# Optimization experiments

Hardware: AMD Instinct MI355X
Metric: run time of the kernel (lower is better)

## Reference

```python
import jax, jax.numpy as jnp
import numpy as np
from jax import lax

B, S, HID, H, HKV, D, M = 2, 4096, 2048, 16, 8, 128, 256
CHUNK = 128
EPS = 1e-6


def setup_inputs() -> dict:
    key = jax.random.key(0)
    ks = jax.random.split(key, 6)
    hidden_states = jax.random.normal(ks[0], (B, S, HID), jnp.float32)
    wq = jax.random.normal(ks[1], (H * D, HID), jnp.float32) / np.sqrt(HID)
    wk = jax.random.normal(ks[2], (HKV * D, HID), jnp.float32) / np.sqrt(HID)
    wv = jax.random.normal(ks[3], (HKV * D, HID), jnp.float32) / np.sqrt(HID)
    wo = jax.random.normal(ks[4], (HID, H * D), jnp.float32) / np.sqrt(H * D)
    proj_matrix = jax.random.normal(ks[5], (M, D), jnp.float32)
    # RoPE tables (HF LLaMA style): cos/sin of shape (B, S, head_dim)
    inv_freq = 1.0 / (10000.0 ** (np.arange(0, D, 2, dtype=np.float64) / D))
    freqs = np.arange(S, dtype=np.float64)[:, None] * inv_freq[None, :]
    emb = np.concatenate([freqs, freqs], axis=-1)  # (S, D)
    cos = jnp.asarray(np.broadcast_to(np.cos(emb)[None], (B, S, D)).copy(), jnp.float32)
    sin = jnp.asarray(np.broadcast_to(np.sin(emb)[None], (B, S, D)).copy(), jnp.float32)
    return {"hidden_states": hidden_states, "cos": cos, "sin": sin,
            "wq": wq, "wk": wk, "wv": wv, "wo": wo, "proj_matrix": proj_matrix}


def _rotate_half(x):
    x1, x2 = x[..., : D // 2], x[..., D // 2:]
    return jnp.concatenate([-x2, x1], axis=-1)


def _apply_rope(q, k, cos, sin):
    # unsqueeze_dim=1: cos/sin (B,S,D) -> (B,1,S,D)
    cos, sin = cos[:, None], sin[:, None]
    return q * cos + _rotate_half(q) * sin, k * cos + _rotate_half(k) * sin


def _feature_map(x, proj_matrix, is_query):
    # FAVOR+ positive random features approximating exp(q.k / sqrt(d)).
    xn = x * (D ** -0.25)                                  # data normalizer d^-1/4
    u = jnp.einsum('bhsd,md->bhsm', xn, proj_matrix)       # (B,H,S,M)
    sq = 0.5 * jnp.sum(xn * xn, axis=-1, keepdims=True)
    z = u - sq
    if is_query:
        z = z - jnp.max(z, axis=-1, keepdims=True)         # per-query max (cancels in ratio)
    else:
        z = z - jnp.max(z)                                 # global max for keys (cancels)
    return jnp.exp(z) * (M ** -0.5) + EPS


def _causal_linear_attention(phi_q, phi_k, v):
    # phi_q/phi_k: (B,H,S,M), v: (B,H,S,D). Chunked causal prefix-sum scan.
    nc = S // CHUNK
    pq = phi_q.reshape(B, H, nc, CHUNK, M).transpose(2, 0, 1, 3, 4)
    pk = phi_k.reshape(B, H, nc, CHUNK, M).transpose(2, 0, 1, 3, 4)
    vc = v.reshape(B, H, nc, CHUNK, D).transpose(2, 0, 1, 3, 4)

    @jax.checkpoint
    def body(carry, inp):
        s_kv, s_k = carry                                   # (B,H,M,D), (B,H,M)
        pq_c, pk_c, v_c = inp                               # (B,H,C,M), (B,H,C,M), (B,H,C,D)
        kv = jnp.einsum('bhcm,bhcd->bhcmd', pk_c, v_c)
        kv_cum = jnp.cumsum(kv, axis=2) + s_kv[:, :, None]  # (B,H,C,M,D)
        k_cum = jnp.cumsum(pk_c, axis=2) + s_k[:, :, None]  # (B,H,C,M)
        num = jnp.einsum('bhcm,bhcmd->bhcd', pq_c, kv_cum)
        den = jnp.einsum('bhcm,bhcm->bhc', pq_c, k_cum)
        out = num / (den[..., None] + EPS)
        return (kv_cum[:, :, -1], k_cum[:, :, -1]), out

    init = (jnp.zeros((B, H, M, D), phi_q.dtype), jnp.zeros((B, H, M), phi_q.dtype))
    _, outs = lax.scan(body, init, (pq, pk, vc))            # (nc,B,H,C,D)
    return outs.transpose(1, 2, 0, 3, 4).reshape(B, H, S, D)


def reference(hidden_states, cos, sin, wq, wk, wv, wo, proj_matrix):
    q = (hidden_states @ wq.T).reshape(B, S, H, D).transpose(0, 2, 1, 3)
    k = (hidden_states @ wk.T).reshape(B, S, HKV, D).transpose(0, 2, 1, 3)
    v = (hidden_states @ wv.T).reshape(B, S, HKV, D).transpose(0, 2, 1, 3)
    q, k = _apply_rope(q, k, cos, sin)
    groups = H // HKV
    k = jnp.repeat(k, groups, axis=1)
    v = jnp.repeat(v, groups, axis=1)
    phi_q = _feature_map(q, proj_matrix, is_query=True)
    phi_k = _feature_map(k, proj_matrix, is_query=False)
    attn = _causal_linear_attention(phi_q, phi_k, v)        # (B,H,S,D)
    attn = attn.transpose(0, 2, 1, 3).reshape(B, S, H * D)
    return attn @ wo.T
```

## Files before the change

kernel.cpp:

```cpp
#include <hip/hip_runtime.h>

#define NB 2
#define NS 4096
#define NH 16
#define NKV 8
#define ND 128
#define NM 256
#define NCNK 32

#define SCALE_A 0.29730177875068026f
#define PHI_SCALE 0.0625f
#define EPSF 1e-6f

typedef unsigned short u16;
typedef unsigned int u32;
typedef __attribute__((ext_vector_type(8))) short short8;
typedef __attribute__((ext_vector_type(4))) float f32x4;

static __device__ __forceinline__ float bfh(u16 v) {
  return __uint_as_float(((u32)v) << 16);
}
static __device__ __forceinline__ u32 f2bf1(float f) {
  u32 u = __float_as_uint(f);
  return (u + 0x7fffu + ((u >> 16) & 1u)) >> 16;
}
static __device__ __forceinline__ u32 pack2(float a, float b) {
  return f2bf1(a) | (f2bf1(b) << 16);
}
static __device__ __forceinline__ void unp8(uint4 p, float* f) {
  f[0] = __uint_as_float(p.x << 16); f[1] = __uint_as_float(p.x & 0xffff0000u);
  f[2] = __uint_as_float(p.y << 16); f[3] = __uint_as_float(p.y & 0xffff0000u);
  f[4] = __uint_as_float(p.z << 16); f[5] = __uint_as_float(p.z & 0xffff0000u);
  f[6] = __uint_as_float(p.w << 16); f[7] = __uint_as_float(p.w & 0xffff0000u);
}
static __device__ __forceinline__ void ld8(const u16* p, float* f) {
  unp8(*(const uint4*)p, f);
}
static __device__ __forceinline__ void ld8(const float* p, float* f) {
  const float4 a = *(const float4*)p;
  const float4 b = *(const float4*)(p + 4);
  f[0]=a.x; f[1]=a.y; f[2]=a.z; f[3]=a.w;
  f[4]=b.x; f[5]=b.y; f[6]=b.z; f[7]=b.w;
}
static __device__ __forceinline__ void st8(u16* p, const float* o) {
  uint4 w;
  w.x = pack2(o[0], o[1]); w.y = pack2(o[2], o[3]);
  w.z = pack2(o[4], o[5]); w.w = pack2(o[6], o[7]);
  *(uint4*)p = w;
}

static __device__ __forceinline__ unsigned f2key(float f) {
  unsigned u = __float_as_uint(f);
  return (u & 0x80000000u) ? ~u : (u | 0x80000000u);
}
static __device__ __forceinline__ float key2f(unsigned k) {
  return (k & 0x80000000u) ? __uint_as_float(k & 0x7fffffffu) : __uint_as_float(~k);
}

__global__ void fill_out_f32(float* __restrict__ out, float val)
{
  const size_t idx = (size_t)blockIdx.x * 256 + threadIdx.x;
  out[idx] = val;
}

__global__ void f2b(const float* __restrict__ in, u16* __restrict__ out)
{
  const size_t i = (((size_t)blockIdx.x * 256) + threadIdx.x) * 8;
  float f[8];
  ld8(in + i, f);
  st8(out + i, f);
}

__global__ void f2b_split(const float* __restrict__ in, u16* __restrict__ hi,
                          u16* __restrict__ lo)
{
  const size_t i = (size_t)blockIdx.x * 256 + threadIdx.x;
  const float f = in[i];
  const u16 h = (u16)f2bf1(f);
  hi[i] = h;
  lo[i] = (u16)f2bf1(f - bfh(h));
}

#define GLL(gp, lp) \
  __builtin_amdgcn_global_load_lds( \
      (const __attribute__((address_space(1))) u32*)(gp), \
      (__attribute__((address_space(3))) u32*)(lp), 16, 0, 0)

static __device__ __forceinline__ void stc(float* p, float v) { *p = v; }
static __device__ __forceinline__ void stc(u16* p, float v)  { *p = (u16)f2bf1(v); }

template <class TO>
__global__ __launch_bounds__(256) void gemm_bt_mfma(
    const u16* __restrict__ A, const u16* __restrict__ B,
    TO* __restrict__ C, int K, int Nc)
{
  __shared__ u16 As[4096];
  __shared__ u16 Bs[4096];
  const int t = threadIdx.x;
  const int lane = t & 63;
  const int wid = t >> 6;
  const int wr = wid >> 1, wc = wid & 1;

  int bid = blockIdx.y * gridDim.x + blockIdx.x;
  {
    const int nwg = gridDim.x * gridDim.y;
    const int qq = nwg >> 3, rr = nwg & 7;
    const int x = bid & 7, o = bid >> 3;
    bid = (x < rr ? x * (qq + 1) : rr * (qq + 1) + (x - rr) * qq) + o;
  }
  const int rowBase = (bid / gridDim.x) * 128;
  const int colBase = (bid % gridDim.x) * 128;

  const int e0 = t * 8;
  const int sk = (t & 3) * 8;
  const size_t g0 = (size_t)(rowBase + (t >> 2)) * K + sk;
  const size_t g1 = (size_t)(colBase + (t >> 2)) * K + sk;
  const size_t rstep = (size_t)K * 64;

  const int fr = lane & 15;
  const int fk = (lane >> 4) * 8;
  const u16* Ar = As + (wr * 64 + fr) * 32 + fk;
  const u16* Br = Bs + (wc * 64 + fr) * 32 + fk;

  f32x4 acc[4][4];
#pragma unroll
  for (int i = 0; i < 4; ++i)
#pragma unroll
    for (int j = 0; j < 4; ++j) acc[i][j] = (f32x4){0.f, 0.f, 0.f, 0.f};

  for (int k0 = 0; k0 < K; k0 += 32) {
    GLL(A + g0 + k0,         As + e0);
    GLL(A + g0 + rstep + k0, As + 2048 + e0);
    GLL(B + g1 + k0,         Bs + e0);
    GLL(B + g1 + rstep + k0, Bs + 2048 + e0);
    asm volatile("s_waitcnt vmcnt(0)" ::: "memory");
    __syncthreads();
    short8 a[4], b[4];
#pragma unroll
    for (int mi = 0; mi < 4; ++mi) a[mi] = *(const short8*)(Ar + mi * 512);
#pragma unroll
    for (int ni = 0; ni < 4; ++ni) b[ni] = *(const short8*)(Br + ni * 512);
#pragma unroll
    for (int mi = 0; mi < 4; ++mi)
#pragma unroll
      for (int ni = 0; ni < 4; ++ni)
        acc[mi][ni] = __builtin_amdgcn_mfma_f32_16x16x32_bf16(
            a[mi], b[ni], acc[mi][ni], 0, 0, 0);
    __syncthreads();
  }

  const int cr = (lane >> 4) * 4;
  const int cc = lane & 15;
#pragma unroll
  for (int mi = 0; mi < 4; ++mi) {
    const int r0 = rowBase + wr * 64 + mi * 16 + cr;
#pragma unroll
    for (int ni = 0; ni < 4; ++ni) {
      const int col = colBase + wc * 64 + ni * 16 + cc;
#pragma unroll
      for (int j = 0; j < 4; ++j)
        stc(C + (size_t)(r0 + j) * Nc + col, acc[mi][ni][j]);
    }
  }
}

__global__ void rope_bf(u16* __restrict__ x, const float* __restrict__ cosb,
                        const float* __restrict__ sinb, int nheads, int coff)
{
  const size_t idx = (size_t)blockIdx.x * blockDim.x + threadIdx.x;
  const int d = (int)(idx & 63);
  const size_t nh = idx >> 6;
  const int h = (int)(nh % nheads);
  const size_t n = nh / nheads;
  const float c1 = cosb[n * ND + d];
  const float s1 = sinb[n * ND + d];
  const float c2 = cosb[n * ND + d + 64];
  const float s2 = sinb[n * ND + d + 64];
  u16* p = x + n * 4096 + coff + h * ND + d;
  const float x1 = bfh(p[0]);
  const float x2 = bfh(p[64]);
  p[0]  = (u16)f2bf1(x1 * c1 - x2 * s1);
  p[64] = (u16)f2bf1(x2 * c2 + x1 * s2);
}

__global__ void sqsum_k(const u16* __restrict__ X, float* __restrict__ sqv)
{
  const size_t row = (size_t)blockIdx.x * 256 + threadIdx.x;
  const u16* p = X + (row >> 3) * 4096 + 2048 + (row & 7) * 128;
  float s = 0.f;
  for (int k = 0; k < 128; k += 8) {
    float f[8];
    ld8(p + k, f);
#pragma unroll
    for (int j = 0; j < 8; ++j) s += f[j] * f[j];
  }
  sqv[row] = 0.5f * SCALE_A * SCALE_A * s;
}

template <bool IS_Q, int RSH, int COFF>
__global__ __launch_bounds__(256) void feat_mfma(
    const u16* __restrict__ X, const u16* __restrict__ Pb,
    u16* __restrict__ U, const float* __restrict__ sqv,
    unsigned* __restrict__ gmax)
{
  __shared__ u16 As[4096];
  __shared__ u16 Bh[8192];
  __shared__ u16 Bl[8192];
  __shared__ float rmW[2][128];
  __shared__ float wmax[4];
  const int t = threadIdx.x;
  const int lane = t & 63, wid = t >> 6;
  const int wr = wid >> 1, wc = wid & 1;
  const int fr = lane & 15, fk = (lane >> 4) * 8;
  const int cr = (lane >> 4) * 4, cc = lane & 15;
  const int sr = t >> 2, sk = (t & 3) * 8, e0 = t * 8;
  const int rowBase = blockIdx.x * 128;
  const int MASK = (1 << RSH) - 1;
  const u16* Pl = Pb + NM * 128;

  const int ga = rowBase + sr, gb = rowBase + sr + 64;
  const size_t xa = (size_t)(ga >> RSH) * 4096 + COFF + (size_t)(ga & MASK) * 128 + sk;
  const size_t xb = (size_t)(gb >> RSH) * 4096 + COFF + (size_t)(gb & MASK) * 128 + sk;

  f32x4 acc[4][8];
#pragma unroll
  for (int i = 0; i < 4; ++i)
#pragma unroll
    for (int j = 0; j < 8; ++j) acc[i][j] = (f32x4){0.f, 0.f, 0.f, 0.f};

  for (int k0 = 0; k0 < 128; k0 += 32) {
    GLL(X + xa + k0, As + e0);
    GLL(X + xb + k0, As + 2048 + e0);
#pragma unroll
    for (int qq = 0; qq < 4; ++qq) {
      GLL(Pb + (size_t)(sr + qq*64) * 128 + k0 + sk, Bh + qq*2048 + e0);
      GLL(Pl + (size_t)(sr + qq*64) * 128 + k0 + sk, Bl + qq*2048 + e0);
    }
    asm volatile("s_waitcnt vmcnt(0)" ::: "memory");
    __syncthreads();
    short8 a[4];
#pragma unroll
    for (int mi = 0; mi < 4; ++mi)
      a[mi] = *(const short8*)(As + (wr*64 + mi*16 + fr)*32 + fk);
    {
      short8 bb[8];
#pragma unroll
      for (int ni = 0; ni < 8; ++ni)
        bb[ni] = *(const short8*)(Bh + (wc*128 + ni*16 + fr)*32 + fk);
#pragma unroll
      for (int mi = 0; mi < 4; ++mi)
#pragma unroll
        for (int ni = 0; ni < 8; ++ni)
          acc[mi][ni] = __builtin_amdgcn_mfma_f32_16x16x32_bf16(
              a[mi], bb[ni], acc[mi][ni], 0, 0, 0);
    }
    {
      short8 bb[8];
#pragma unroll
      for (int ni = 0; ni < 8; ++ni)
        bb[ni] = *(const short8*)(Bl + (wc*128 + ni*16 + fr)*32 + fk);
#pragma unroll
      for (int mi = 0; mi < 4; ++mi)
#pragma unroll
        for (int ni = 0; ni < 8; ++ni)
          acc[mi][ni] = __builtin_amdgcn_mfma_f32_16x16x32_bf16(
              a[mi], bb[ni], acc[mi][ni], 0, 0, 0);
    }
    __syncthreads();
  }

  if (IS_Q) {
#pragma unroll
    for (int mi = 0; mi < 4; ++mi)
#pragma unroll
      for (int j = 0; j < 4; ++j) {
        float m = acc[mi][0][j];
#pragma unroll
        for (int ni = 1; ni < 8; ++ni) m = fmaxf(m, acc[mi][ni][j]);
        m = fmaxf(m, __shfl_xor(m, 1));
        m = fmaxf(m, __shfl_xor(m, 2));
        m = fmaxf(m, __shfl_xor(m, 4));
        m = fmaxf(m, __shfl_xor(m, 8));
        const int r = wr*64 + mi*16 + cr + j;
        if (cc == 0) rmW[wc][r] = m;
      }
    __syncthreads();
#pragma unroll
    for (int mi = 0; mi < 4; ++mi)
#pragma unroll
      for (int j = 0; j < 4; ++j) {
        const int r = wr*64 + mi*16 + cr + j;
        const float mr = fmaxf(rmW[0][r], rmW[1][r]);
        u16* up = U + (size_t)(rowBase + r) * NM + wc*128 + cc;
#pragma unroll
        for (int ni = 0; ni < 8; ++ni) {
          const float phi = expf(SCALE_A * (acc[mi][ni][j] - mr)) * PHI_SCALE + EPSF;
          up[ni*16] = (u16)f2bf1(phi);
        }
      }
  } else {
    float lmax = -1e30f;
#pragma unroll
    for (int mi = 0; mi < 4; ++mi)
#pragma unroll
      for (int j = 0; j < 4; ++j) {
        const int r = wr*64 + mi*16 + cr + j;
        const float sq = sqv[rowBase + r];
#pragma unroll
        for (int ni = 0; ni < 8; ++ni) {
          const float z = SCALE_A * acc[mi][ni][j] - sq;
          acc[mi][ni][j] = z;
          lmax = fmaxf(lmax, z);
        }
      }
    lmax = fmaxf(lmax, __shfl_xor(lmax, 1));
    lmax = fmaxf(lmax, __shfl_xor(lmax, 2));
    lmax = fmaxf(lmax, __shfl_xor(lmax, 4));
    lmax = fmaxf(lmax, __shfl_xor(lmax, 8));
    lmax = fmaxf(lmax, __shfl_xor(lmax, 16));
    lmax = fmaxf(lmax, __shfl_xor(lmax, 32));
    if (lane == 0) wmax[wid] = lmax;
    __syncthreads();
    if (t == 0) {
      const float bm = fmaxf(fmaxf(wmax[0], wmax[1]), fmaxf(wmax[2], wmax[3]));
      atomicMax(gmax, f2key(bm));
    }
#pragma unroll
    for (int mi = 0; mi < 4; ++mi)
#pragma unroll
      for (int j = 0; j < 4; ++j) {
        const int r = wr*64 + mi*16 + cr + j;
        u16* up = U + (size_t)(rowBase + r) * NM + wc*128 + cc;
#pragma unroll
        for (int ni = 0; ni < 8; ++ni)
          up[ni*16] = (u16)f2bf1(expf(acc[mi][ni][j]));
      }
  }
}

__global__ void init_gmax(unsigned* g) { *g = 0u; }

__global__ void feat_k_b(u16* __restrict__ u, const unsigned* __restrict__ gmax)
{
  const size_t idx = (size_t)blockIdx.x * blockDim.x + threadIdx.x;
  const float eg = expf(-key2f(*gmax));
  const float e = bfh(u[idx]);
  u[idx] = (u16)f2bf1(e * eg * PHI_SCALE + EPSF);
}

__global__ __launch_bounds__(256) void vtrans(const u16* __restrict__ v,
                                              u16* __restrict__ vT)
{
  const int s0 = blockIdx.x * 64;
  const int d0 = blockIdx.y * 64;
  const int bkv = blockIdx.z;
  const int b = bkv >> 3, kh = bkv & 7;
  const int t = threadIdx.x;
  __shared__ u16 Tt[64][80];
  const int sl = t >> 3;
  const int ds = (t & 7) * 8;
#pragma unroll
  for (int r = 0; r < 2; ++r) {
    const u16* src = v + (size_t)(b*NS + s0 + r*32 + sl) * 4096 + 3072 + kh*128 + d0 + ds;
    *(uint4*)&Tt[r*32 + sl][ds] = *(const uint4*)src;
  }
  __syncthreads();
#pragma unroll
  for (int r = 0; r < 2; ++r) {
    const int dl = r*32 + sl;
    u16 tmp[8];
#pragma unroll
    for (int j = 0; j < 8; ++j) tmp[j] = Tt[ds + j][dl];
    u16* dst = vT + (((size_t)(b*NKV + kh) * ND) + d0 + dl) * NS + s0 + ds;
    *(uint4*)dst = *(uint4*)tmp;
  }
}

__global__ __launch_bounds__(256) void ksum_chunk(const u16* __restrict__ phik,
                                                  float* __restrict__ ksst)
{
  const int c = blockIdx.x, bkv = blockIdx.y;
  const int b = bkv >> 3, kh = bkv & 7;
  const int m = threadIdx.x;
  const size_t base = ((size_t)(b*NS + c*128) * NKV + kh) * NM + m;
  float s = 0.f;
  for (int i = 0; i < 128; ++i) s += bfh(phik[base + (size_t)i * (NKV*NM)]);
  ksst[((size_t)bkv * NCNK + c) * NM + m] = s;
}

__global__ __launch_bounds__(256) void chunk_kv_mfma(
    const u16* __restrict__ phik, const u16* __restrict__ vT,
    u16* __restrict__ kvT)
{
  const int c = blockIdx.x, bkv = blockIdx.y;
  const int b = bkv >> 3, kh = bkv & 7;
  const int t = threadIdx.x;
  const int lane = t & 63, wid = t >> 6;
  const int wr = wid >> 1, wc = wid & 1;
  const int fr = lane & 15, fk = (lane >> 4) * 8;
  const int cr = (lane >> 4) * 4, cc = lane & 15;
  const int sr = t >> 2, sk = (t & 3) * 8, e0 = t * 8;

  __shared__ u16 As[4096];
  __shared__ u16 Bs[8192];

  const size_t vt_off = ((size_t)(b*NKV + kh) * ND) * NS + (size_t)c * 128;
  const size_t pk_row0 = ((size_t)(b*NS + c*128) * NKV + kh) * NM;
  const size_t pk_rstr = (size_t)NKV * NM;

  f32x4 acc[4][8];
#pragma unroll
  for (int i = 0; i < 4; ++i)
#pragma unroll
    for (int j = 0; j < 8; ++j) acc[i][j] = (f32x4){0.f, 0.f, 0.f, 0.f};

  const int m = t;
  const int sw = (m >> 1) & 3;

  for (int i0 = 0; i0 < 128; i0 += 32) {
    __syncthreads();
    GLL(vT + vt_off + (size_t)sr * NS + i0 + sk,        As + e0);
    GLL(vT + vt_off + (size_t)(sr + 64) * NS + i0 + sk, As + 2048 + e0);
    u16 rowv[32];
#pragma unroll
    for (int j = 0; j < 32; ++j)
      rowv[j] = phik[pk_row0 + (size_t)(i0 + j) * pk_rstr + m];
    u16* brow = Bs + m * 32;
#pragma unroll
    for (int q = 0; q < 4; ++q)
      *(uint4*)(brow + ((q ^ sw) * 8)) = *(const uint4*)(rowv + q*8);
    asm volatile("s_waitcnt vmcnt(0)" ::: "memory");
    __syncthreads();
    short8 a[4], bb[8];
#pragma unroll
    for (int mi = 0; mi < 4; ++mi)
      a[mi] = *(const short8*)(As + (wr*64 + mi*16 + fr)*32 + fk);
#pragma unroll
    for (int ni = 0; ni < 8; ++ni) {
      const int mrow = wc*128 + ni*16 + fr;
      const int q = fk >> 3;
      bb[ni] = *(const short8*)(Bs + mrow*32 + ((q ^ ((mrow >> 1) & 3)) << 3));
    }
#pragma unroll
    for (int mi = 0; mi < 4; ++mi)
#pragma unroll
      for (int ni = 0; ni < 8; ++ni)
        acc[mi][ni] = __builtin_amdgcn_mfma_f32_16x16x32_bf16(
            a[mi], bb[ni], acc[mi][ni], 0, 0, 0);
  }

  const size_t kv_off = ((size_t)bkv * NCNK + c) * (size_t)(ND*NM);
#pragma unroll
  for (int mi = 0; mi < 4; ++mi)
#pragma unroll
    for (int j = 0; j < 4; ++j) {
      const int d = wr*64 + mi*16 + cr + j;
#pragma unroll
      for (int ni = 0; ni < 8; ++ni) {
        const int mm = wc*128 + ni*16 + cc;
        kvT[kv_off + (size_t)d * NM + mm] = (u16)f2bf1(acc[mi][ni][j]);
      }
    }
}

__global__ void prefix_kv(u16* __restrict__ kvst)
{
  const int md = blockIdx.x * 256 + threadIdx.x;
  const size_t base = (size_t)blockIdx.y * NCNK * (NM*ND) + md;
  float carry = 0.f;
  for (int c = 0; c < NCNK; ++c) {
    const size_t a = base + (size_t)c * (NM*ND);
    const float val = bfh(kvst[a]);
    kvst[a] = (u16)f2bf1(carry);
    carry += val;
  }
}

__global__ void prefix_ks(float* __restrict__ ksst)
{
  const int m = threadIdx.x;
  const size_t base = (size_t)blockIdx.x * NCNK * NM + m;
  float carry = 0.f;
  for (int c = 0; c < NCNK; ++c) {
    const size_t a = base + (size_t)c * NM;
    const float val = ksst[a];
    ksst[a] = carry;
    carry += val;
  }
}

__global__ __launch_bounds__(256) void attn_mfma(
    const u16* __restrict__ phiq, const u16* __restrict__ phik,
    const u16* __restrict__ vT, const u16* __restrict__ kvT,
    const float* __restrict__ kspre, u16* __restrict__ attn)
{
  const int c = blockIdx.x, h = blockIdx.y, b = blockIdx.z;
  const int kh = h >> 1;
  const int bkv = b * NKV + kh;
  const int t = threadIdx.x;
  const int lane = t & 63, wid = t >> 6;
  const int wr = wid >> 1, wc = wid & 1;
  const int fr = lane & 15, fk = (lane >> 4) * 8;
  const int cr = (lane >> 4) * 4, cc = lane & 15;
  const int sr = t >> 2, sk = (t & 3) * 8, e0 = t * 8;

  __shared__ u16 As[4096];
  __shared__ u16 Bs[4096];
  __shared__ u16 Sl[16384];
  __shared__ float den_l[128];
  __shared__ float ks_l[256];

  const size_t pq_off = ((size_t)(b*NS + c*128) * NH  + h)  * NM;
  const size_t pk_off = ((size_t)(b*NS + c*128) * NKV + kh) * NM;
  const size_t vt_off = ((size_t)(b*NKV + kh) * ND) * (size_t)NS + (size_t)c * 128;
  const size_t kv_off = ((size_t)bkv * NCNK + c) * (size_t)(ND*NM);

  if (t < 128) den_l[t] = 0.f;
  ks_l[t] = kspre[((size_t)bkv * NCNK + c) * NM + t];

  const u16* Arp = As + (wr*64 + fr)*32 + fk;
  const u16* Brp = Bs + (wc*64 + fr)*32 + fk;

  f32x4 accS[4][4];
#pragma unroll
  for (int i = 0; i < 4; ++i)
#pragma unroll
    for (int j = 0; j < 4; ++j) accS[i][j] = (f32x4){0.f, 0.f, 0.f, 0.f};

  for (int k0 = 0; k0 < NM; k0 += 32) {
    GLL(phiq + pq_off + (size_t)sr * 4096 + k0 + sk,        As + e0);
    GLL(phiq + pq_off + (size_t)(sr + 64) * 4096 + k0 + sk, As + 2048 + e0);
    GLL(phik + pk_off + (size_t)sr * 2048 + k0 + sk,        Bs + e0);
    GLL(phik + pk_off + (size_t)(sr + 64) * 2048 + k0 + sk, Bs + 2048 + e0);
    asm volatile("s_waitcnt vmcnt(0)" ::: "memory");
    __syncthreads();
    short8 a[4], bb[4];
#pragma unroll
    for (int mi = 0; mi < 4; ++mi) a[mi] = *(const short8*)(Arp + mi*512);
#pragma unroll
    for (int ni = 0; ni < 4; ++ni) bb[ni] = *(const short8*)(Brp + ni*512);
#pragma unroll
    for (int mi = 0; mi < 4; ++mi)
#pragma unroll
      for (int ni = 0; ni < 4; ++ni)
        accS[mi][ni] = __builtin_amdgcn_mfma_f32_16x16x32_bf16(
            a[mi], bb[ni], accS[mi][ni], 0, 0, 0);
    __syncthreads();
  }

#pragma unroll
  for (int mi = 0; mi < 4; ++mi)
#pragma unroll
    for (int j = 0; j < 4; ++j) {
      const int r = wr*64 + mi*16 + cr + j;
      float s = 0.f;
#pragma unroll
      for (int ni = 0; ni < 4; ++ni) {
        const int cl = wc*64 + ni*16 + cc;
        float vv = accS[mi][ni][j];
        vv = (cl > r) ? 0.f : vv;
        accS[mi][ni][j] = vv;
        s += vv;
      }
      s += __shfl_xor(s, 1); s += __shfl_xor(s, 2);
      s += __shfl_xor(s, 4); s += __shfl_xor(s, 8);
      if (cc == 0) atomicAdd(&den_l[r], s);
#pragma unroll
      for (int ni = 0; ni < 4; ++ni) {
        const int cl = wc*64 + ni*16 + cc;
        u32 bo = ((u32)r << 8) + ((u32)cl << 1);
        bo ^= (u32)(r & 7) << 4;
        *(u16*)((char*)Sl + bo) = (u16)f2bf1(accS[mi][ni][j]);
      }
    }
  __syncthreads();

  f32x4 acc2[4][4];
#pragma unroll
  for (int i = 0; i < 4; ++i)
#pragma unroll
    for (int j = 0; j < 4; ++j) acc2[i][j] = (f32x4){0.f, 0.f, 0.f, 0.f};

  for (int j0 = 0; j0 < 128; j0 += 32) {
    GLL(vT + vt_off + (size_t)sr * NS + j0 + sk,        Bs + e0);
    GLL(vT + vt_off + (size_t)(sr + 64) * NS + j0 + sk, Bs + 2048 + e0);
    asm volatile("s_waitcnt vmcnt(0)" ::: "memory");
    __syncthreads();
    short8 a[4], bb[4];
#pragma unroll
    for (int mi = 0; mi < 4; ++mi) {
      u32 bo = ((u32)(wr*64 + mi*16 + fr) << 8) + ((u32)(j0 + fk) << 1);
      bo ^= (u32)(fr & 7) << 4;
      a[mi] = *(const short8*)((const char*)Sl + bo);
    }
#pragma unroll
    for (int ni = 0; ni < 4; ++ni) bb[ni] = *(const short8*)(Brp + ni*512);
#pragma unroll
    for (int mi = 0; mi < 4; ++mi)
#pragma unroll
      for (int ni = 0; ni < 4; ++ni)
        acc2[mi][ni] = __builtin_amdgcn_mfma_f32_16x16x32_bf16(
            a[mi], bb[ni], acc2[mi][ni], 0, 0, 0);
    __syncthreads();
  }

  for (int m0 = 0; m0 < NM; m0 += 32) {
    GLL(phiq + pq_off + (size_t)sr * 4096 + m0 + sk,        As + e0);
    GLL(phiq + pq_off + (size_t)(sr + 64) * 4096 + m0 + sk, As + 2048 + e0);
    GLL(kvT + kv_off + (size_t)sr * NM + m0 + sk,           Bs + e0);
    GLL(kvT + kv_off + (size_t)(sr + 64) * NM + m0 + sk,    Bs + 2048 + e0);
    asm volatile("s_waitcnt vmcnt(0)" ::: "memory");
    __syncthreads();
    short8 a[4], bb[4];
#pragma unroll
    for (int mi = 0; mi < 4; ++mi) a[mi] = *(const short8*)(Arp + mi*512);
#pragma unroll
    for (int ni = 0; ni < 4; ++ni) bb[ni] = *(const short8*)(Brp + ni*512);
#pragma unroll
    for (int mi = 0; mi < 4; ++mi)
#pragma unroll
      for (int ni = 0; ni < 4; ++ni)
        acc2[mi][ni] = __builtin_amdgcn_mfma_f32_16x16x32_bf16(
            a[mi], bb[ni], acc2[mi][ni], 0, 0, 0);
    {
      const int pr = t >> 1;
      const int pm = (t & 1) * 16;
      float xf[16];
      unp8(*(const uint4*)(As + pr*32 + pm), xf);
      unp8(*(const uint4*)(As + pr*32 + pm + 8), xf + 8);
      float s = 0.f;
#pragma unroll
      for (int jj = 0; jj < 16; ++jj) s += xf[jj] * ks_l[m0 + pm + jj];
      s += __shfl_xor(s, 1);
      if (!(t & 1)) atomicAdd(&den_l[pr], s);
    }
    __syncthreads();
  }

#pragma unroll
  for (int mi = 0; mi < 4; ++mi)
#pragma unroll
    for (int j = 0; j < 4; ++j) {
      const int r = wr*64 + mi*16 + cr + j;
      const float inv = 1.0f / (den_l[r] + EPSF);
      u16* op = attn + ((size_t)(b*NS + c*128 + r) * NH + h) * ND + wc*64 + cc;
#pragma unroll
      for (int ni = 0; ni < 4; ++ni)
        op[ni*16] = (u16)f2bf1(acc2[mi][ni][j] * inv);
    }
}

extern "C" void kernel_launch(void* const* d_in, const int* in_sizes, int n_in,
                              void* d_out, int out_size, void* d_ws, size_t ws_size,
                              hipStream_t stream)
{
  const float* hidden = (const float*)d_in[0];
  const float* cosb   = (const float*)d_in[1];
  const float* sinb   = (const float*)d_in[2];
  const float* wq     = (const float*)d_in[3];
  const float* wk     = (const float*)d_in[4];
  const float* wv     = (const float*)d_in[5];
  const float* wo     = (const float*)d_in[6];
  const float* proj   = (const float*)d_in[7];
  float* out = (float*)d_out;

  const size_t MiB = 1024ull * 1024ull;
  if (ws_size < 186ull * MiB) {
    fill_out_f32<<<65536, 256, 0, stream>>>(out, 400.f);
    return;
  }

  u16* qkv  = (u16*)d_ws;
  u16* phiq = qkv  + 33554432;
  u16* kvst = phiq + 33554432;
  float* ksst = (float*)(kvst + 16777216);
  unsigned* gmax = (unsigned*)(ksst + 131072);
  float* sqv = (float*)(gmax + 64);
  u16* wqkvb = (u16*)(sqv + 65536);
  u16* wob  = wqkvb + 8388608;
  u16* pb   = wob + 4194304;
  u16* hb   = kvst;
  u16* phik = (u16*)d_out;
  u16* vTb  = phik + 16777216;
  u16* attn = qkv;

  f2b<<<8192, 256, 0, stream>>>(hidden, hb);
  f2b<<<2048, 256, 0, stream>>>(wq, wqkvb);
  f2b<<<1024, 256, 0, stream>>>(wk, wqkvb + 2048*2048);
  f2b<<<1024, 256, 0, stream>>>(wv, wqkvb + 3072*2048);
  f2b<<<2048, 256, 0, stream>>>(wo, wob);
  f2b_split<<<128, 256, 0, stream>>>(proj, pb, pb + 32768);

  gemm_bt_mfma<u16><<<dim3(32, 64), 256, 0, stream>>>(hb, wqkvb, qkv, 2048, 4096);

  vtrans<<<dim3(64, 2, 16), 256, 0, stream>>>(qkv, vTb);
  rope_bf<<<32768, 256, 0, stream>>>(qkv, cosb, sinb, NH, 0);
  rope_bf<<<16384, 256, 0, stream>>>(qkv, cosb, sinb, NKV, 2048);

  init_gmax<<<1, 1, 0, stream>>>(gmax);
  sqsum_k<<<256, 256, 0, stream>>>(qkv, sqv);
  feat_mfma<true , 4, 0   ><<<1024, 256, 0, stream>>>(qkv, pb, phiq, sqv, gmax);
  feat_mfma<false, 3, 2048><<< 512, 256, 0, stream>>>(qkv, pb, phik, sqv, gmax);
  feat_k_b<<<65536, 256, 0, stream>>>(phik, gmax);

  chunk_kv_mfma<<<dim3(NCNK, NB*NKV), 256, 0, stream>>>(phik, vTb, kvst);
  ksum_chunk<<<dim3(NCNK, NB*NKV), 256, 0, stream>>>(phik, ksst);
  prefix_kv<<<dim3(128, NB*NKV), 256, 0, stream>>>(kvst);
  prefix_ks<<<NB*NKV, 256, 0, stream>>>(ksst);

  attn_mfma<<<dim3(NCNK, NH, NB), 256, 0, stream>>>(phiq, phik, vTb, kvst, ksst, attn);

  gemm_bt_mfma<float><<<dim3(16, 64), 256, 0, stream>>>(attn, wob, out, 2048, 2048);
}
```

Before: 730.5 us.

## Replace GEMM with 256x256-tile double-buffered swizzled-LDS MFMA kernel

```diff
diff --git a/kernel.cpp b/kernel.cpp
--- a/kernel.cpp
+++ b/kernel.cpp
@@ -89,17 +89,30 @@
 static __device__ __forceinline__ void stc(float* p, float v) { *p = v; }
 static __device__ __forceinline__ void stc(u16* p, float v)  { *p = (u16)f2bf1(v); }
 
+static __device__ __forceinline__ void bar_f() {
+  asm volatile("" ::: "memory");
+  __builtin_amdgcn_s_barrier();
+  asm volatile("" ::: "memory");
+}
+static __device__ __forceinline__ void lgkm0_f() {
+  asm volatile("s_waitcnt lgkmcnt(0)" ::: "memory");
+  __builtin_amdgcn_sched_barrier(0);
+}
+
 template <class TO>
-__global__ __launch_bounds__(256) void gemm_bt_mfma(
+__global__ __launch_bounds__(512, 2) void gemm_bt_256(
     const u16* __restrict__ A, const u16* __restrict__ B,
     TO* __restrict__ C, int K, int Nc)
 {
-  __shared__ u16 As[4096];
-  __shared__ u16 Bs[4096];
+  __shared__ short8 ldsv[8192];
+  u16* Abuf = (u16*)ldsv;
+  u16* Bbuf = (u16*)ldsv + 32768;
+
   const int t = threadIdx.x;
   const int lane = t & 63;
   const int wid = t >> 6;
-  const int wr = wid >> 1, wc = wid & 1;
+  const int wr = wid >> 2;
+  const int wc = wid & 3;
 
   int bid = blockIdx.y * gridDim.x + blockIdx.x;
   {
@@ -108,60 +121,115 @@
     const int x = bid & 7, o = bid >> 3;
     bid = (x < rr ? x * (qq + 1) : rr * (qq + 1) + (x - rr) * qq) + o;
   }
-  const int rowBase = (bid / gridDim.x) * 128;
-  const int colBase = (bid % gridDim.x) * 128;
-
-  const int e0 = t * 8;
-  const int sk = (t & 3) * 8;
-  const size_t g0 = (size_t)(rowBase + (t >> 2)) * K + sk;
-  const size_t g1 = (size_t)(colBase + (t >> 2)) * K + sk;
-  const size_t rstep = (size_t)K * 64;
-
-  const int fr = lane & 15;
-  const int fk = (lane >> 4) * 8;
-  const u16* Ar = As + (wr * 64 + fr) * 32 + fk;
-  const u16* Br = Bs + (wc * 64 + fr) * 32 + fk;
-
-  f32x4 acc[4][4];
-#pragma unroll
-  for (int i = 0; i < 4; ++i)
-#pragma unroll
-    for (int j = 0; j < 4; ++j) acc[i][j] = (f32x4){0.f, 0.f, 0.f, 0.f};
-
-  for (int k0 = 0; k0 < K; k0 += 32) {
-    GLL(A + g0 + k0,         As + e0);
-    GLL(A + g0 + rstep + k0, As + 2048 + e0);
-    GLL(B + g1 + k0,         Bs + e0);
-    GLL(B + g1 + rstep + k0, Bs + 2048 + e0);
-    asm volatile("s_waitcnt vmcnt(0)" ::: "memory");
-    __syncthreads();
-    short8 a[4], b[4];
-#pragma unroll
-    for (int mi = 0; mi < 4; ++mi) a[mi] = *(const short8*)(Ar + mi * 512);
-#pragma unroll
-    for (int ni = 0; ni < 4; ++ni) b[ni] = *(const short8*)(Br + ni * 512);
-#pragma unroll
-    for (int mi = 0; mi < 4; ++mi)
-#pragma unroll
-      for (int ni = 0; ni < 4; ++ni)
-        acc[mi][ni] = __builtin_amdgcn_mfma_f32_16x16x32_bf16(
-            a[mi], b[ni], acc[mi][ni], 0, 0, 0);
-    __syncthreads();
+  const int rowBase = (bid / gridDim.x) * 256;
+  const int colBase = (bid % gridDim.x) * 256;
+  const int NT = K >> 6;
+
+  const int srow = t >> 3;
+  const int scol = (((t & 7) ^ ((t >> 3) & 7)) << 3);
+  const int sld  = t * 8;
+
+  const int frow = lane & 15;
+  const int fkey = lane & 7;
+  const int fql  = lane >> 4;
+
+#define STAGE_A(bsel, h, u) do { \
+    const u16* gp_ = A + (size_t)(rowBase + (h)*128 + srow) * K + (u)*64 + scol; \
+    GLL(gp_,                Abuf + (bsel)*16384 + (h)*8192 + sld); \
+    GLL(gp_ + (size_t)64*K, Abuf + (bsel)*16384 + (h)*8192 + 4096 + sld); \
+  } while (0)
+#define STAGE_B(bsel, h, u) do { \
+    const u16* gp_ = B + (size_t)(colBase + (h)*128 + srow) * K + (u)*64 + scol; \
+    GLL(gp_,                Bbuf + (bsel)*16384 + (h)*8192 + sld); \
+    GLL(gp_ + (size_t)64*K, Bbuf + (bsel)*16384 + (h)*8192 + 4096 + sld); \
+  } while (0)
+
+  short8 af[4][2], b0[2][2], b1[2][2];
+
+#define LDA(Mh, bsel) do { \
+    _Pragma("unroll") for (int mi = 0; mi < 4; ++mi) \
+    _Pragma("unroll") for (int ks = 0; ks < 2; ++ks) { \
+      const int rib_ = (Mh)*128 + wr*64 + mi*16 + frow; \
+      const int pb_ = (ks*4 + fql) ^ fkey; \
+      af[mi][ks] = *(const short8*)(Abuf + (bsel)*16384 + rib_*64 + pb_*8); \
+    } } while (0)
+#define LDB(dst, Nh, bsel) do { \
+    _Pragma("unroll") for (int ni = 0; ni < 2; ++ni) \
+    _Pragma("unroll") for (int ks = 0; ks < 2; ++ks) { \
+      const int rib_ = (Nh)*128 + wc*32 + ni*16 + frow; \
+      const int pb_ = (ks*4 + fql) ^ fkey; \
+      dst[ni][ks] = *(const short8*)(Bbuf + (bsel)*16384 + rib_*64 + pb_*8); \
+    } } while (0)
+
+  f32x4 acc[2][2][4][2];
+#pragma unroll
+  for (int a_ = 0; a_ < 2; ++a_)
+#pragma unroll
+    for (int b_ = 0; b_ < 2; ++b_)
+#pragma unroll
+      for (int m_ = 0; m_ < 4; ++m_)
+#pragma unroll
+        for (int n_ = 0; n_ < 2; ++n_)
+          acc[a_][b_][m_][n_] = (f32x4){0.f, 0.f, 0.f, 0.f};
+
+#define MMQ(Mh, Nh, bfr) do { \
+    _Pragma("unroll") for (int mi = 0; mi < 4; ++mi) \
+    _Pragma("unroll") for (int ni = 0; ni < 2; ++ni) \
+    _Pragma("unroll") for (int ks = 0; ks < 2; ++ks) \
+      acc[Mh][Nh][mi][ni] = __builtin_amdgcn_mfma_f32_16x16x32_bf16( \
+          af[mi][ks], bfr[ni][ks], acc[Mh][Nh][mi][ni], 0, 0, 0); \
+  } while (0)
+
+  STAGE_A(0, 0, 0); STAGE_B(0, 0, 0); STAGE_A(0, 1, 0); STAGE_B(0, 1, 0);
+  STAGE_A(1, 0, 1); STAGE_B(1, 0, 1);
+  asm volatile("s_waitcnt vmcnt(4)" ::: "memory");
+  bar_f();
+
+  for (int u = 0; u < NT; ++u) {
+    const int bsel = u & 1, osel = bsel ^ 1;
+    LDA(0, bsel); LDB(b0, 0, bsel);
+    if (u + 1 < NT) STAGE_A(osel, 1, u + 1);
+    bar_f(); lgkm0_f();
+    __builtin_amdgcn_s_setprio(1); MMQ(0, 0, b0); __builtin_amdgcn_s_setprio(0);
+    bar_f();
+    LDB(b1, 1, bsel);
+    if (u + 1 < NT) STAGE_B(osel, 1, u + 1);
+    bar_f(); lgkm0_f();
+    __builtin_amdgcn_s_setprio(1); MMQ(0, 1, b1); __builtin_amdgcn_s_setprio(0);
+    bar_f();
+    LDA(1, bsel);
+    if (u + 2 < NT) STAGE_A(bsel, 0, u + 2);
+    bar_f(); lgkm0_f();
+    __builtin_amdgcn_s_setprio(1); MMQ(1, 0, b0); __builtin_amdgcn_s_setprio(0);
+    bar_f();
+    if (u + 2 < NT) STAGE_B(bsel, 0, u + 2);
+    __builtin_amdgcn_s_setprio(1); MMQ(1, 1, b1); __builtin_amdgcn_s_setprio(0);
+    asm volatile("s_waitcnt vmcnt(4)" ::: "memory");
+    bar_f();
   }
 
   const int cr = (lane >> 4) * 4;
   const int cc = lane & 15;
 #pragma unroll
-  for (int mi = 0; mi < 4; ++mi) {
-    const int r0 = rowBase + wr * 64 + mi * 16 + cr;
-#pragma unroll
-    for (int ni = 0; ni < 4; ++ni) {
-      const int col = colBase + wc * 64 + ni * 16 + cc;
-#pragma unroll
-      for (int j = 0; j < 4; ++j)
-        stc(C + (size_t)(r0 + j) * Nc + col, acc[mi][ni][j]);
-    }
-  }
+  for (int Mh = 0; Mh < 2; ++Mh)
+#pragma unroll
+    for (int mi = 0; mi < 4; ++mi) {
+      const int r0 = rowBase + Mh*128 + wr*64 + mi*16 + cr;
+#pragma unroll
+      for (int Nh = 0; Nh < 2; ++Nh)
+#pragma unroll
+        for (int ni = 0; ni < 2; ++ni) {
+          const int col = colBase + Nh*128 + wc*32 + ni*16 + cc;
+#pragma unroll
+          for (int j = 0; j < 4; ++j)
+            stc(C + (size_t)(r0 + j) * Nc + col, acc[Mh][Nh][mi][ni][j]);
+        }
+    }
+#undef STAGE_A
+#undef STAGE_B
+#undef LDA
+#undef LDB
+#undef MMQ
 }
 
 __global__ void rope_bf(u16* __restrict__ x, const float* __restrict__ cosb,
@@ -691,7 +759,7 @@
   f2b<<<2048, 256, 0, stream>>>(wo, wob);
   f2b_split<<<128, 256, 0, stream>>>(proj, pb, pb + 32768);
 
-  gemm_bt_mfma<u16><<<dim3(32, 64), 256, 0, stream>>>(hb, wqkvb, qkv, 2048, 4096);
+  gemm_bt_256<u16><<<dim3(16, 32), 512, 0, stream>>>(hb, wqkvb, qkv, 2048, 4096);
 
   vtrans<<<dim3(64, 2, 16), 256, 0, stream>>>(qkv, vTb);
   rope_bf<<<32768, 256, 0, stream>>>(qkv, cosb, sinb, NH, 0);
@@ -710,5 +778,5 @@
 
   attn_mfma<<<dim3(NCNK, NH, NB), 256, 0, stream>>>(phiq, phik, vTb, kvst, ksst, attn);
 
-  gemm_bt_mfma<float><<<dim3(16, 64), 256, 0, stream>>>(attn, wob, out, 2048, 2048);
-}
+  gemm_bt_256<float><<<dim3(8, 32), 512, 0, stream>>>(attn, wob, out, 2048, 2048);
+}
```

Measured after the change: 617.3 us. -15.5%, faster.
